# Optimization experiments

Hardware: AMD Instinct MI355X
Metric: run time of the kernel (lower is better)

The kernel has to match this reference:

```python
import jax, jax.numpy as jnp
import numpy as np

SCALE = 0.08838834764831845  # 1/sqrt(output_dim=128)


def setup_inputs() -> dict:
    key = jax.random.key(0)
    ks = jax.random.split(key, 7)
    N, D, H, E = 4096, 1024, 8, 128
    s = 0.02
    return {
        "X": jax.random.normal(ks[0], (N, D), jnp.float32),
        "Wq": jax.random.normal(ks[1], (H, D, E), jnp.float32) * s,
        "bq": jax.random.normal(ks[2], (H, E), jnp.float32) * s,
        "Wk": jax.random.normal(ks[3], (H, D, E), jnp.float32) * s,
        "bk": jax.random.normal(ks[4], (H, E), jnp.float32) * s,
        "Wv": jax.random.normal(ks[5], (H, D, E), jnp.float32) * s,
        "bv": jax.random.normal(ks[6], (H, E), jnp.float32) * s,
    }


def reference(X, Wq, bq, Wk, bk, Wv, bv):
    # per-head projections, batched over heads: [H, N, E]
    q = jnp.einsum("nd,hde->hne", X, Wq) + bq[:, None, :]
    k = jnp.einsum("nd,hde->hne", X, Wk) + bk[:, None, :]
    v = jnp.einsum("nd,hde->hne", X, Wv) + bv[:, None, :]
    # score[h, n, m] = scale * q[h,n,:] . k[h,m,:]  ([H, N, N])
    score = SCALE * jnp.einsum("hne,hme->hnm", q, k)
    # NOTE: original uses nn.Softmax(dim=0) on the [N, N] per-head matrix,
    # i.e. normalization over the QUERY (row) axis -> axis=1 here.
    attn = jax.nn.softmax(score, axis=1)
    # z[h, n, e] = sum_m attn[h,n,m] * v[h,m,e]
    z = jnp.einsum("hnm,hme->hne", attn, v)
    # concat heads along feature dim: [N, H*E]
    H, N, E = z.shape
    Z = jnp.transpose(z, (1, 0, 2)).reshape(N, H * E)
    return jax.nn.sigmoid(Z)
```

## Files before the change

kernel.cpp:

```cpp
#include <hip/hip_runtime.h>
#include <hip/hip_bf16.h>
#include <stdint.h>

typedef __bf16 bf16_t;
typedef __bf16 bf16x4 __attribute__((ext_vector_type(4)));
typedef __bf16 bf16x8 __attribute__((ext_vector_type(8)));
typedef float f32x4 __attribute__((ext_vector_type(4)));

#define MFMA_16x16x32(A, B, C) __builtin_amdgcn_mfma_f32_16x16x32_bf16(A, B, C, 0, 0, 0)
#define EXP2(x) __builtin_amdgcn_exp2f(x)

static constexpr float kScale = 0.08838834764831845f;
static constexpr float kLog2e = 1.4426950408889634f;
static constexpr float kC1 = kScale * kLog2e;

__device__ __forceinline__ void lds_cp16(void* lds, const void* g) {
  __builtin_amdgcn_global_load_lds(
      (__attribute__((address_space(1))) void*)(uintptr_t)g,
      (__attribute__((address_space(3))) void*)(uintptr_t)lds, 16, 0, 0);
}

template <int R, int K>
__device__ __forceinline__ void stage_tile(bf16_t* lds, const bf16_t* g, int ldg, int tid) {
  constexpr int TOT = R * K;
  constexpr int CH = R * 32;
  constexpr int ITERS = TOT / 2048;
  const int wave = tid >> 6;
#pragma unroll
  for (int i = 0; i < ITERS; ++i) {
    int linear = i * 2048 + tid * 8;
    int chunk = linear / CH;
    int rem = linear % CH;
    int r = rem >> 5;
    int c = rem & 31;
    lds_cp16(lds + i * 2048 + wave * 512, g + r * ldg + chunk * 32 + c);
  }
}

__device__ __forceinline__ bf16x8 frag_ld(const bf16_t* lds_chunk, int row, int lane) {
  return *(const bf16x8*)(lds_chunk + row * 32 + ((lane >> 4) << 3));
}

__global__ void cvt_kernel(const float* __restrict__ src, bf16_t* __restrict__ dst) {
  const int i = (blockIdx.x * 256 + threadIdx.x) * 4;
  float4 v = *(const float4*)&src[i];
  bf16x4 o;
  o[0] = (bf16_t)v.x;
  o[1] = (bf16_t)v.y;
  o[2] = (bf16_t)v.z;
  o[3] = (bf16_t)v.w;
  *(bf16x4*)&dst[i] = o;
}

__global__ void transpose_f32_k(const float* __restrict__ src, bf16_t* __restrict__ dst, int R,
                                int C) {
  __shared__ alignas(16) bf16_t tile[64][72];
  const int t = threadIdx.x;
  const int mat = blockIdx.z;
  const int r0 = blockIdx.x * 64, c0 = blockIdx.y * 64;
  const float* s = src + (size_t)mat * R * C;
  bf16_t* d = dst + (size_t)mat * R * C;
  const int rl = t >> 3, cl = (t & 7) * 8;
#pragma unroll
  for (int half = 0; half < 2; ++half) {
    const int r = r0 + rl + half * 32;
    float4 a = *(const float4*)&s[(size_t)r * C + c0 + cl];
    float4 b = *(const float4*)&s[(size_t)r * C + c0 + cl + 4];
    tile[cl + 0][rl + half * 32] = (bf16_t)a.x;
    tile[cl + 1][rl + half * 32] = (bf16_t)a.y;
    tile[cl + 2][rl + half * 32] = (bf16_t)a.z;
    tile[cl + 3][rl + half * 32] = (bf16_t)a.w;
    tile[cl + 4][rl + half * 32] = (bf16_t)b.x;
    tile[cl + 5][rl + half * 32] = (bf16_t)b.y;
    tile[cl + 6][rl + half * 32] = (bf16_t)b.z;
    tile[cl + 7][rl + half * 32] = (bf16_t)b.w;
  }
  __syncthreads();
  const int cl2 = t >> 3, rl2 = (t & 7) * 8;
  *(bf16x8*)&d[(size_t)(c0 + cl2) * R + r0 + rl2] = *(const bf16x8*)&tile[cl2][rl2];
  *(bf16x8*)&d[(size_t)(c0 + cl2 + 32) * R + r0 + rl2] = *(const bf16x8*)&tile[cl2 + 32][rl2];
}

__global__ __launch_bounds__(256, 2) void proj_kernel(const bf16_t* __restrict__ X,
                                                      const bf16_t* __restrict__ Wt,
                                                      const float* __restrict__ bq,
                                                      const float* __restrict__ bk,
                                                      const float* __restrict__ bv,
                                                      bf16_t* __restrict__ qkv) {
  __shared__ alignas(16) char smem[34816];
  bf16_t* As = (bf16_t*)smem;
  bf16_t* Bs = (bf16_t*)(smem + 8192);
  const int t = threadIdx.x, lane = t & 63, w = t >> 6;
  const int l15 = lane & 15, quad = lane >> 4;
  const int ntile = blockIdx.x, mat = blockIdx.y;
  const bf16_t* a0 = X + (size_t)ntile * 128 * 1024;
  const bf16_t* b0 = Wt + (size_t)mat * 131072;
  f32x4 acc[4][4] = {};
  const int rb = (w >> 1) * 64, cb = (w & 1) * 64;
  for (int k0 = 0; k0 < 1024; k0 += 32) {
    stage_tile<128, 32>(As, a0 + k0, 1024, t);
    stage_tile<128, 32>(Bs, b0 + k0, 1024, t);
    __syncthreads();
    bf16x8 af[4], bfr[4];
#pragma unroll
    for (int i = 0; i < 4; ++i) af[i] = frag_ld(As, rb + i * 16 + l15, lane);
#pragma unroll
    for (int j = 0; j < 4; ++j) bfr[j] = frag_ld(Bs, cb + j * 16 + l15, lane);
#pragma unroll
    for (int i = 0; i < 4; ++i)
#pragma unroll
      for (int j = 0; j < 4; ++j) acc[i][j] = MFMA_16x16x32(af[i], bfr[j], acc[i][j]);
    __syncthreads();
  }
  const int proj = mat >> 3, h = mat & 7;
  const float* bias = (proj == 0 ? bq : proj == 1 ? bk : bv) + h * 128;
  bf16_t* Ct = (bf16_t*)smem;
  bf16_t* dst = qkv + (size_t)proj * 4194304 + (size_t)h * 524288;
  if (proj < 2) {
#pragma unroll
    for (int i = 0; i < 4; ++i)
#pragma unroll
      for (int j = 0; j < 4; ++j) {
        const int e = cb + j * 16 + l15;
        const float bval = bias[e];
#pragma unroll
        for (int r = 0; r < 4; ++r)
          Ct[(rb + i * 16 + quad * 4 + r) * 136 + e] = (bf16_t)(acc[i][j][r] + bval);
      }
    __syncthreads();
#pragma unroll
    for (int u = 0; u < 2; ++u) {
      const int nt = w * 2 + u;
#pragma unroll
      for (int ks = 0; ks < 4; ++ks) {
        bf16x8 f = *(const bf16x8*)&Ct[(nt * 16 + l15) * 136 + ks * 32 + quad * 8];
        *(bf16x8*)&dst[(((size_t)(ntile * 8 + nt)) * 4 + ks) * 512 + lane * 8] = f;
      }
    }
  } else {
#pragma unroll
    for (int i = 0; i < 4; ++i)
#pragma unroll
      for (int j = 0; j < 4; ++j) {
        const int e = cb + j * 16 + l15;
        const float bval = bias[e];
        bf16x4 pv;
#pragma unroll
        for (int r = 0; r < 4; ++r) pv[r] = (bf16_t)(acc[i][j][r] + bval);
        *(bf16x4*)&Ct[e * 136 + rb + i * 16 + quad * 4] = pv;
      }
    __syncthreads();
#pragma unroll
    for (int es = 0; es < 8; ++es) {
      bf16x8 f = *(const bf16x8*)&Ct[(es * 16 + l15) * 136 + w * 32 + quad * 8];
      *(bf16x8*)&dst[(((size_t)(ntile * 4 + w)) * 8 + es) * 512 + lane * 8] = f;
    }
  }
}

__global__ __launch_bounds__(256, 2) void pass_a_kernel(const bf16_t* __restrict__ Qf,
                                                        const bf16_t* __restrict__ Kf,
                                                        float* __restrict__ l2c) {
  __shared__ alignas(16) float csred[4][64];
  const int t = threadIdx.x, lane = t & 63, w = t >> 6;
  const int l15 = lane & 15;
  const int h = blockIdx.x, mtile = blockIdx.y;
  const bf16_t* Qh = Qf + (size_t)h * 524288;
  const bf16_t* Kh = Kf + (size_t)h * 524288;
  bf16x8 kf[16];
#pragma unroll
  for (int mg = 0; mg < 4; ++mg)
#pragma unroll
    for (int ks = 0; ks < 4; ++ks)
      kf[mg * 4 + ks] = *(const bf16x8*)&Kh[((mtile * 4 + mg) * 4 + ks) * 512 + lane * 8];
  float cs[4] = {0.f, 0.f, 0.f, 0.f};
  uint32_t qo = w * 2048 + lane * 8;
  bf16x8 af[4];
#pragma unroll
  for (int ks = 0; ks < 4; ++ks) af[ks] = *(const bf16x8*)&Qh[qo + ks * 512];
  for (int it = 0; it < 64; ++it) {
    f32x4 c[4] = {};
#pragma unroll
    for (int ks = 0; ks < 4; ++ks)
#pragma unroll
      for (int mg = 0; mg < 4; ++mg) c[mg] = MFMA_16x16x32(af[ks], kf[mg * 4 + ks], c[mg]);
    qo += 8192;
#pragma unroll
    for (int ks = 0; ks < 4; ++ks) af[ks] = *(const bf16x8*)&Qh[qo + ks * 512];
#pragma unroll
    for (int mg = 0; mg < 4; ++mg)
#pragma unroll
      for (int r = 0; r < 4; ++r) cs[mg] += EXP2(c[mg][r] * kC1);
  }
#pragma unroll
  for (int mg = 0; mg < 4; ++mg) {
    cs[mg] += __shfl_xor(cs[mg], 16, 64);
    cs[mg] += __shfl_xor(cs[mg], 32, 64);
  }
  if (lane < 16) {
#pragma unroll
    for (int mg = 0; mg < 4; ++mg) csred[w][mg * 16 + lane] = cs[mg];
  }
  __syncthreads();
  if (t < 64)
    l2c[(size_t)h * 4096 + mtile * 64 + t] =
        __builtin_log2f(csred[0][t] + csred[1][t] + csred[2][t] + csred[3][t]);
}

__global__ __launch_bounds__(512, 2) void pass_b_kernel(const bf16_t* __restrict__ Qf,
                                                        const bf16_t* __restrict__ Kf,
                                                        const bf16_t* __restrict__ Vf,
                                                        const float* __restrict__ l2c,
                                                        float* __restrict__ out) {
  __shared__ alignas(16) char smem[86016];
  const int t = threadIdx.x, lane = t & 63, w = t >> 6;
  const int quad = lane >> 4, l15 = lane & 15;
  const int npar = w & 3, mpar = w >> 2;
  const int h = blockIdx.x, ntile = blockIdx.y;
  const char* KhB = (const char*)(Kf + (size_t)h * 524288);
  const char* VhB = (const char*)(Vf + (size_t)h * 524288);
  const bf16_t* Qh = Qf + (size_t)h * 524288;
  const float* lb = l2c + (size_t)h * 4096;
  bf16_t* sW = (bf16_t*)(smem + 65536) + w * 1280;

#pragma unroll
  for (int j = 0; j < 2; ++j) {
    const int off = (w * 2 + j) * 1024;
    lds_cp16(smem + off, KhB + off + lane * 16);
    lds_cp16(smem + 16384 + off, VhB + off + lane * 16);
  }
  bf16x8 qf[2][4];
#pragma unroll
  for (int nsub = 0; nsub < 2; ++nsub)
#pragma unroll
    for (int ks = 0; ks < 4; ++ks)
      qf[nsub][ks] =
          *(const bf16x8*)&Qh[((ntile * 8 + npar * 2 + nsub) * 4 + ks) * 512 + lane * 8];
  f32x4 zacc[2][8] = {};
  __syncthreads();

  for (int it = 0; it < 64; ++it) {
    const int cur = it & 1;
    if (it < 63) {
      char* kdst = smem + (cur ^ 1) * 32768;
      const char* ksrc = KhB + (size_t)(it + 1) * 16384;
      const char* vsrc = VhB + (size_t)(it + 1) * 16384;
#pragma unroll
      for (int j = 0; j < 2; ++j) {
        const int off = (w * 2 + j) * 1024;
        lds_cp16(kdst + off, ksrc + off + lane * 16);
        lds_cp16(kdst + 16384 + off, vsrc + off + lane * 16);
      }
    }
    const int st = it * 2 + mpar;
    f32x4 g0 = *(const f32x4*)&lb[st * 32 + quad * 4];
    f32x4 g1 = *(const f32x4*)&lb[st * 32 + 16 + quad * 4];
    const bf16_t* kbase = (const bf16_t*)(smem + cur * 32768) + mpar * 4096;
    bf16x8 kf[8];
#pragma unroll
    for (int u = 0; u < 8; ++u) kf[u] = *(const bf16x8*)&kbase[u * 512 + lane * 8];
    f32x4 cc[2][2] = {};
#pragma unroll
    for (int ks = 0; ks < 4; ++ks)
#pragma unroll
      for (int ms = 0; ms < 2; ++ms)
#pragma unroll
        for (int nsub = 0; nsub < 2; ++nsub)
          cc[ms][nsub] = MFMA_16x16x32(kf[ms * 4 + ks], qf[nsub][ks], cc[ms][nsub]);
#pragma unroll
    for (int ms = 0; ms < 2; ++ms) {
      const f32x4 g = ms ? g1 : g0;
#pragma unroll
      for (int nsub = 0; nsub < 2; ++nsub) {
        bf16x4 pv;
#pragma unroll
        for (int r = 0; r < 4; ++r) pv[r] = (bf16_t)EXP2(cc[ms][nsub][r] * kC1 - g[r]);
        *(bf16x4*)&sW[(nsub * 16 + l15) * 40 + ms * 16 + quad * 4] = pv;
      }
    }
    bf16x8 pf[2];
#pragma unroll
    for (int nsub = 0; nsub < 2; ++nsub)
      pf[nsub] = *(const bf16x8*)&sW[(nsub * 16 + l15) * 40 + quad * 8];
    const bf16_t* vbase = (const bf16_t*)(smem + cur * 32768 + 16384) + mpar * 4096;
#pragma unroll
    for (int es = 0; es < 8; ++es) {
      bf16x8 vf = *(const bf16x8*)&vbase[es * 512 + lane * 8];
#pragma unroll
      for (int nsub = 0; nsub < 2; ++nsub)
        zacc[nsub][es] = MFMA_16x16x32(pf[nsub], vf, zacc[nsub][es]);
    }
    __syncthreads();
  }
  float* red = (float*)smem;
  if (mpar == 1) {
#pragma unroll
    for (int nsub = 0; nsub < 2; ++nsub)
#pragma unroll
      for (int es = 0; es < 8; ++es)
        *(f32x4*)&red[npar * 4096 + (nsub * 8 + es) * 256 + lane * 4] = zacc[nsub][es];
  }
  __syncthreads();
  if (mpar == 0) {
#pragma unroll
    for (int nsub = 0; nsub < 2; ++nsub) {
#pragma unroll
      for (int es = 0; es < 8; ++es) {
        f32x4 o = *(const f32x4*)&red[npar * 4096 + (nsub * 8 + es) * 256 + lane * 4];
        const int e = es * 16 + l15;
#pragma unroll
        for (int r = 0; r < 4; ++r) {
          const int n = ntile * 128 + npar * 32 + nsub * 16 + quad * 4 + r;
          const float z = zacc[nsub][es][r] + o[r];
          out[(size_t)n * 1024 + h * 128 + e] = 1.f / (1.f + EXP2(-z * kLog2e));
        }
      }
    }
  }
}

extern "C" void kernel_launch(void* const* d_in, const int* in_sizes, int n_in, void* d_out,
                              int out_size, void* d_ws, size_t ws_size, hipStream_t stream) {
  (void)in_sizes;
  (void)n_in;
  (void)out_size;
  (void)ws_size;
  const float* X = (const float*)d_in[0];
  const float* Wq = (const float*)d_in[1];
  const float* bq = (const float*)d_in[2];
  const float* Wk = (const float*)d_in[3];
  const float* bk = (const float*)d_in[4];
  const float* Wv = (const float*)d_in[5];
  const float* bv = (const float*)d_in[6];
  float* out = (float*)d_out;
  char* ws = (char*)d_ws;
  bf16_t* Qf = (bf16_t*)(ws);
  bf16_t* Kf = (bf16_t*)(ws + 8388608);
  bf16_t* Vf = (bf16_t*)(ws + 16777216);
  bf16_t* Xb = (bf16_t*)(ws + 25165824);
  bf16_t* Wt = (bf16_t*)(ws + 33554432);
  float* l2c = (float*)(ws + 39845888);

  cvt_kernel<<<4096, 256, 0, stream>>>(X, Xb);
  transpose_f32_k<<<dim3(16, 2, 8), 256, 0, stream>>>(Wq, Wt + (size_t)0 * 8 * 131072, 1024, 128);
  transpose_f32_k<<<dim3(16, 2, 8), 256, 0, stream>>>(Wk, Wt + (size_t)1 * 8 * 131072, 1024, 128);
  transpose_f32_k<<<dim3(16, 2, 8), 256, 0, stream>>>(Wv, Wt + (size_t)2 * 8 * 131072, 1024, 128);
  proj_kernel<<<dim3(32, 24), 256, 0, stream>>>(Xb, Wt, bq, bk, bv, Qf);
  pass_a_kernel<<<dim3(8, 64), 256, 0, stream>>>(Qf, Kf, l2c);
  pass_b_kernel<<<dim3(8, 32), 512, 0, stream>>>(Qf, Kf, Vf, l2c, out);
}
```

Baseline: 248.4 us.

## Merge weight transposes, raise pass_a occupancy, stream V via registers

The three weight-transpose launches become one launch that picks Wq/Wk/Wv from blockIdx.z. pass_a's launch bounds go from 2 to 4 blocks per CU and its main loop is kept rolled, to raise occupancy. In pass_b, V tiles are no longer staged through LDS. Each wave loads its V fragments straight from global memory into registers, prefetching one iteration ahead, so the LDS double buffer holds only K. This cuts LDS traffic and footprint but raises register pressure in pass_b and makes each wave issue uncoalesced-per-block global loads for V.

```diff
diff --git a/kernel.cpp b/kernel.cpp
--- a/kernel.cpp
+++ b/kernel.cpp
@@ -52,13 +52,14 @@
   *(bf16x4*)&dst[i] = o;
 }
 
-__global__ void transpose_f32_k(const float* __restrict__ src, bf16_t* __restrict__ dst, int R,
-                                int C) {
+__global__ void transpose_w_kernel(const float* __restrict__ Wq, const float* __restrict__ Wk,
+                                   const float* __restrict__ Wv, bf16_t* __restrict__ dst) {
   __shared__ alignas(16) bf16_t tile[64][72];
   const int t = threadIdx.x;
   const int mat = blockIdx.z;
+  constexpr int R = 1024, C = 128;
   const int r0 = blockIdx.x * 64, c0 = blockIdx.y * 64;
-  const float* s = src + (size_t)mat * R * C;
+  const float* s = (mat < 8 ? Wq : mat < 16 ? Wk : Wv) + (size_t)(mat & 7) * R * C;
   bf16_t* d = dst + (size_t)mat * R * C;
   const int rl = t >> 3, cl = (t & 7) * 8;
 #pragma unroll
@@ -158,7 +159,7 @@
   }
 }
 
-__global__ __launch_bounds__(256, 2) void pass_a_kernel(const bf16_t* __restrict__ Qf,
+__global__ __launch_bounds__(256, 4) void pass_a_kernel(const bf16_t* __restrict__ Qf,
                                                         const bf16_t* __restrict__ Kf,
                                                         float* __restrict__ l2c) {
   __shared__ alignas(16) float csred[4][64];
@@ -178,6 +179,7 @@
   bf16x8 af[4];
 #pragma unroll
   for (int ks = 0; ks < 4; ++ks) af[ks] = *(const bf16x8*)&Qh[qo + ks * 512];
+#pragma unroll 1
   for (int it = 0; it < 64; ++it) {
     f32x4 c[4] = {};
 #pragma unroll
@@ -218,16 +220,15 @@
   const int npar = w & 3, mpar = w >> 2;
   const int h = blockIdx.x, ntile = blockIdx.y;
   const char* KhB = (const char*)(Kf + (size_t)h * 524288);
-  const char* VhB = (const char*)(Vf + (size_t)h * 524288);
+  const bf16_t* Vh = Vf + (size_t)h * 524288;
   const bf16_t* Qh = Qf + (size_t)h * 524288;
   const float* lb = l2c + (size_t)h * 4096;
   bf16_t* sW = (bf16_t*)(smem + 65536) + w * 1280;
 
 #pragma unroll
   for (int j = 0; j < 2; ++j) {
-    const int off = (w * 2 + j) * 1024;
+    const int off = w * 2048 + j * 1024;
     lds_cp16(smem + off, KhB + off + lane * 16);
-    lds_cp16(smem + 16384 + off, VhB + off + lane * 16);
   }
   bf16x8 qf[2][4];
 #pragma unroll
@@ -236,26 +237,32 @@
     for (int ks = 0; ks < 4; ++ks)
       qf[nsub][ks] =
           *(const bf16x8*)&Qh[((ntile * 8 + npar * 2 + nsub) * 4 + ks) * 512 + lane * 8];
+  uint32_t vo = mpar * 4096 + lane * 8;
+  bf16x8 vf[8];
+#pragma unroll
+  for (int es = 0; es < 8; ++es) vf[es] = *(const bf16x8*)&Vh[vo + es * 512];
   f32x4 zacc[2][8] = {};
   __syncthreads();
 
   for (int it = 0; it < 64; ++it) {
     const int cur = it & 1;
     if (it < 63) {
-      char* kdst = smem + (cur ^ 1) * 32768;
+      char* kdst = smem + (cur ^ 1) * 16384;
       const char* ksrc = KhB + (size_t)(it + 1) * 16384;
-      const char* vsrc = VhB + (size_t)(it + 1) * 16384;
 #pragma unroll
       for (int j = 0; j < 2; ++j) {
-        const int off = (w * 2 + j) * 1024;
+        const int off = w * 2048 + j * 1024;
         lds_cp16(kdst + off, ksrc + off + lane * 16);
-        lds_cp16(kdst + 16384 + off, vsrc + off + lane * 16);
-      }
-    }
+      }
+    }
+    vo += 8192;
+    bf16x8 vfn[8];
+#pragma unroll
+    for (int es = 0; es < 8; ++es) vfn[es] = *(const bf16x8*)&Vh[vo + es * 512];
     const int st = it * 2 + mpar;
     f32x4 g0 = *(const f32x4*)&lb[st * 32 + quad * 4];
     f32x4 g1 = *(const f32x4*)&lb[st * 32 + 16 + quad * 4];
-    const bf16_t* kbase = (const bf16_t*)(smem + cur * 32768) + mpar * 4096;
+    const bf16_t* kbase = (const bf16_t*)(smem + cur * 16384) + mpar * 4096;
     bf16x8 kf[8];
 #pragma unroll
     for (int u = 0; u < 8; ++u) kf[u] = *(const bf16x8*)&kbase[u * 512 + lane * 8];
@@ -282,14 +289,13 @@
 #pragma unroll
     for (int nsub = 0; nsub < 2; ++nsub)
       pf[nsub] = *(const bf16x8*)&sW[(nsub * 16 + l15) * 40 + quad * 8];
-    const bf16_t* vbase = (const bf16_t*)(smem + cur * 32768 + 16384) + mpar * 4096;
-#pragma unroll
-    for (int es = 0; es < 8; ++es) {
-      bf16x8 vf = *(const bf16x8*)&vbase[es * 512 + lane * 8];
+#pragma unroll
+    for (int es = 0; es < 8; ++es)
 #pragma unroll
       for (int nsub = 0; nsub < 2; ++nsub)
-        zacc[nsub][es] = MFMA_16x16x32(pf[nsub], vf, zacc[nsub][es]);
-    }
+        zacc[nsub][es] = MFMA_16x16x32(pf[nsub], vf[es], zacc[nsub][es]);
+#pragma unroll
+    for (int es = 0; es < 8; ++es) vf[es] = vfn[es];
     __syncthreads();
   }
   float* red = (float*)smem;
@@ -342,9 +348,7 @@
   float* l2c = (float*)(ws + 39845888);
 
   cvt_kernel<<<4096, 256, 0, stream>>>(X, Xb);
-  transpose_f32_k<<<dim3(16, 2, 8), 256, 0, stream>>>(Wq, Wt + (size_t)0 * 8 * 131072, 1024, 128);
-  transpose_f32_k<<<dim3(16, 2, 8), 256, 0, stream>>>(Wk, Wt + (size_t)1 * 8 * 131072, 1024, 128);
-  transpose_f32_k<<<dim3(16, 2, 8), 256, 0, stream>>>(Wv, Wt + (size_t)2 * 8 * 131072, 1024, 128);
+  transpose_w_kernel<<<dim3(16, 2, 24), 256, 0, stream>>>(Wq, Wk, Wv, Wt);
   proj_kernel<<<dim3(32, 24), 256, 0, stream>>>(Xb, Wt, bq, bk, bv, Qf);
   pass_a_kernel<<<dim3(8, 64), 256, 0, stream>>>(Qf, Kf, l2c);
   pass_b_kernel<<<dim3(8, 32), 512, 0, stream>>>(Qf, Kf, Vf, l2c, out);
```

Measured after the change: 249.2 us. About the same (+0.3%).
